# Performance work log

Hardware: AMD Instinct MI355X
Metric: run time of the kernel (lower is better)

## Reference

```python
import jax, jax.numpy as jnp
import numpy as np

DIST_THRESH = 0.1
W_DIST = 0.05
W_CHAMFER = 0.05
W_SEP = 0.0005


def setup_inputs() -> dict:
    key = jax.random.key(0)
    k1, k2, k3, k4 = jax.random.split(key, 4)
    B, N, K = 4, 200000, 64
    return {
        "landmarks_C": jax.random.uniform(k1, (B, N, 3), jnp.float32),          # predicted point coords
        "landmarks_F": jax.random.normal(k2, (B, N, 4), jnp.float32) * 0.05,    # [dist, dx, dy, dz]
        "targets_C": jax.random.uniform(k3, (B, K, 3), jnp.float32),            # GT landmark coords
        "targets_F": jax.random.randint(k4, (B, K), 0, 8),                      # GT landmark class labels
        "classes": jnp.arange(6),                                               # classes to supervise
    }


def reference(landmarks_C, landmarks_F, targets_C, targets_F, classes):
    def per_batch(C_i, F_i, tC, tF):
        # class mask over GT landmarks (replaces boolean indexing in torch)
        mask_k = jnp.any(tF[None, :] == classes[:, None], axis=0)          # [K]
        n_valid = mask_k.sum()
        dists_i = F_i[:, 0]                                                # predicted distance, [N]
        coords_i = C_i + F_i[:, 1:]                                        # refined coords, [N,3]
        # pairwise dists GT landmarks -> raw point coords, invalid classes pushed to +inf
        pd = jnp.linalg.norm(C_i[None, :, :] - tC[:, None, :], axis=-1)    # [K,N]
        pd = jnp.where(mask_k[:, None], pd, jnp.inf)
        min_d = pd.min(axis=0)                                             # [N]
        pm = min_d < DIST_THRESH                                           # points near some GT landmark
        # smooth-L1 (beta=1, sum) on predicted distance; clip(inf)=2*thresh reproduces empty-target fallback
        tgt = jnp.clip(min_d, 0.0, 2.0 * DIST_THRESH)
        diff = dists_i - tgt
        ad = jnp.abs(diff)
        dist_loss = jnp.where(ad < 1.0, 0.5 * diff * diff, ad - 0.5).sum()
        # pairwise dists GT landmarks -> refined coords
        ld = jnp.linalg.norm(coords_i[None, :, :] - tC[:, None, :], axis=-1)  # [K,N]
        ld_m = jnp.where(mask_k[:, None], ld, jnp.inf)
        p2g = jnp.where(pm, ld_m.min(axis=0), 0.0)                         # pred->gt, masked points only
        g2p = jnp.where(mask_k, ld_m.min(axis=1), 0.0)                     # gt->pred, valid GT only
        chamfer = (p2g * p2g).sum() + (g2p * g2p).sum()
        # separation: ratio of dists to 2 nearest (valid) GT landmarks, per masked point
        _, idx = jax.lax.top_k(-pd.T, 2)                                   # [N,2] indices of 2 smallest
        d01 = jnp.take_along_axis(ld.T, idx, axis=1)                       # [N,2]
        sep = jnp.where(pm, d01[:, 0] / d01[:, 1], 0.0).sum()
        sep = jnp.where(n_valid >= 2, sep, 0.0)
        return W_DIST * dist_loss + W_CHAMFER * chamfer + W_SEP * sep

    losses = jax.vmap(per_batch)(landmarks_C, landmarks_F, targets_C, targets_F)
    return losses.mean()
```

## Files before the change

kernel.cpp:

```cpp
#include <hip/hip_runtime.h>


constexpr int KT = 64;
constexpr int P  = 2;
constexpr float DIST_THRESH = 0.1f;
constexpr float W_DIST    = 0.05f;
constexpr float W_CHAMFER = 0.05f;
constexpr float W_SEP     = 0.0005f;
constexpr float PT_SENT = 1e18f;
constexpr float TG_SENT = -1e18f;
constexpr float BIGF = 3.0e38f;

__global__ void init_ws_kernel(unsigned int* g2p, float* sums, int ng, int ns) {
    int t = blockIdx.x * blockDim.x + threadIdx.x;
    if (t < ng) g2p[t] = 0x7F7FFFFFu;
    if (t < ns) sums[t] = 0.0f;
}

__global__ __launch_bounds__(256, 2)
void landmark_main(const float* __restrict__ C, const float* __restrict__ F,
                   const float* __restrict__ tC, const int* __restrict__ tF,
                   const int* __restrict__ classes, int n_classes,
                   int B, int N, int blocks_per_batch, int chunks_per_batch,
                   unsigned int* __restrict__ g2p_ws, float* __restrict__ sums)
{
    __shared__ float tx[KT], ty[KT], tz[KT];
    __shared__ float gredw[4][KT];
    __shared__ float rs[3][4];

    const int tid  = threadIdx.x;
    const int lane = tid & 63;
    const int wib  = tid >> 6;
    const int b    = blockIdx.x / blocks_per_batch;
    const int waves_per_batch = blocks_per_batch * (blockDim.x >> 6);
    const int wid  = (blockIdx.x - b * blocks_per_batch) * (blockDim.x >> 6) + wib;

    if (tid < KT) {
        int f = tF[b * KT + tid];
        bool valid = false;
        for (int c = 0; c < n_classes; ++c) valid = valid || (f == classes[c]);
        float x = TG_SENT, y = TG_SENT, z = TG_SENT;
        if (valid) {
            x = tC[(b * KT + tid) * 3 + 0];
            y = tC[(b * KT + tid) * 3 + 1];
            z = tC[(b * KT + tid) * 3 + 2];
        }
        tx[tid] = x; ty[tid] = y; tz[tid] = z;
    }
    __syncthreads();

    const float*  Cb = C + (size_t)b * N * 3;
    const float4* Fb = (const float4*)(F + (size_t)b * N * 4);

    float gmin = BIGF;
    float dist_acc = 0.f, p2g_acc = 0.f, sep_acc = 0.f;

    for (int chunk = wid; chunk < chunks_per_batch; chunk += waves_per_batch) {
        const int base = chunk * (64 * P);

        float px[P], py[P], pz[P], cx[P], cy[P], cz[P], f0[P];
        bool  vp[P];
        #pragma unroll
        for (int p = 0; p < P; ++p) {
            int n = base + p * 64 + lane;
            bool v = (n < N);
            vp[p] = v;
            int ni = v ? n : 0;
            float4 f4 = Fb[ni];
            float X = Cb[3 * ni + 0], Y = Cb[3 * ni + 1], Z = Cb[3 * ni + 2];
            f0[p] = f4.x;
            if (v) {
                px[p] = X;           py[p] = Y;           pz[p] = Z;
                cx[p] = X + f4.y;    cy[p] = Y + f4.z;    cz[p] = Z + f4.w;
            } else {
                px[p] = PT_SENT; py[p] = PT_SENT; pz[p] = PT_SENT;
                cx[p] = PT_SENT; cy[p] = PT_SENT; cz[p] = PT_SENT;
            }
        }

        float m1[P], m2[P], l1[P], l2[P], lmin[P];
        #pragma unroll
        for (int p = 0; p < P; ++p) {
            m1[p] = BIGF; m2[p] = BIGF; l1[p] = BIGF; l2[p] = BIGF; lmin[p] = BIGF;
        }

        int kk = lane;
        #pragma unroll 8
        for (int i = 0; i < 64; ++i) {
            float Tx = tx[kk], Ty = ty[kk], Tz = tz[kk];
            float dl = BIGF;
            #pragma unroll
            for (int p = 0; p < P; ++p) {
                float dx = px[p] - Tx, dy = py[p] - Ty, dz = pz[p] - Tz;
                float pd2 = fmaf(dz, dz, fmaf(dy, dy, dx * dx));
                float ex = cx[p] - Tx, ey = cy[p] - Ty, ez = cz[p] - Tz;
                float ld2 = fmaf(ez, ez, fmaf(ey, ey, ex * ex));
                bool c1 = pd2 < m1[p];
                bool c2 = pd2 < m2[p];
                m2[p] = c1 ? m1[p] : (c2 ? pd2 : m2[p]);
                l2[p] = c1 ? l1[p] : (c2 ? ld2 : l2[p]);
                m1[p] = c1 ? pd2 : m1[p];
                l1[p] = c1 ? ld2 : l1[p];
                lmin[p] = fminf(lmin[p], ld2);
                dl = fminf(dl, ld2);
            }
            float got = __shfl(dl, (lane - i) & 63, 64);
            gmin = fminf(gmin, got);
            kk = (kk + 1) & 63;
        }

        #pragma unroll
        for (int p = 0; p < P; ++p) {
            float mind = sqrtf(m1[p]);
            bool pm = mind < DIST_THRESH;
            float tgt = fminf(mind, 2.0f * DIST_THRESH);
            float diff = f0[p] - tgt;
            float ad = fabsf(diff);
            float sl1 = (ad < 1.0f) ? 0.5f * diff * diff : (ad - 0.5f);
            if (vp[p]) dist_acc += sl1;
            if (pm) {
                p2g_acc += lmin[p];
                sep_acc += sqrtf(l1[p]) / sqrtf(l2[p]);
            }
        }
    }

    float v0 = dist_acc, v1 = p2g_acc, v2 = sep_acc;
    #pragma unroll
    for (int o = 32; o > 0; o >>= 1) {
        v0 += __shfl_down(v0, o, 64);
        v1 += __shfl_down(v1, o, 64);
        v2 += __shfl_down(v2, o, 64);
    }
    if (lane == 0) { rs[0][wib] = v0; rs[1][wib] = v1; rs[2][wib] = v2; }
    gredw[wib][lane] = gmin;
    __syncthreads();

    const int nw = blockDim.x >> 6;
    if (tid < 3) {
        float s = 0.f;
        for (int w = 0; w < nw; ++w) s += rs[tid][w];
        atomicAdd(&sums[tid * B + b], s);
    }
    if (tid < KT) {
        float g = gredw[0][tid];
        for (int w = 1; w < nw; ++w) g = fminf(g, gredw[w][tid]);
        atomicMin(&g2p_ws[b * KT + tid], __float_as_uint(g));
    }
}

__global__ void landmark_finalize(const int* __restrict__ tF, const int* __restrict__ classes,
                                  int n_classes, const unsigned int* __restrict__ g2p_ws,
                                  const float* __restrict__ sums, float* __restrict__ out, int B)
{
    int tid = threadIdx.x;
    int b = tid >> 6, k = tid & 63;
    __shared__ float lossb[32];
    float g = 0.f, nv = 0.f;
    if (b < B) {
        int f = tF[b * KT + k];
        bool valid = false;
        for (int c = 0; c < n_classes; ++c) valid = valid || (f == classes[c]);
        if (valid) { nv = 1.f; g = __uint_as_float(g2p_ws[b * KT + k]); }
    }
    #pragma unroll
    for (int o = 32; o > 0; o >>= 1) {
        g  += __shfl_down(g, o, 64);
        nv += __shfl_down(nv, o, 64);
    }
    if (b < B && k == 0) {
        float sep = (nv >= 2.f) ? sums[2 * B + b] : 0.f;
        lossb[b] = W_DIST * sums[b] + W_CHAMFER * (sums[B + b] + g) + W_SEP * sep;
    }
    __syncthreads();
    if (tid == 0) {
        float s = 0.f;
        for (int i = 0; i < B; ++i) s += lossb[i];
        out[0] = s / (float)B;
    }
}

extern "C" void kernel_launch(void* const* d_in, const int* in_sizes, int n_in,
                              void* d_out, int out_size, void* d_ws, size_t ws_size,
                              hipStream_t stream)
{
    const float* C       = (const float*)d_in[0];
    const float* F       = (const float*)d_in[1];
    const float* tC      = (const float*)d_in[2];
    const int*   tF      = (const int*)d_in[3];
    const int*   classes = (const int*)d_in[4];
    const int n_classes = in_sizes[4];
    const int B = 4;
    const int N = in_sizes[0] / (3 * B);

    unsigned int* g2p_ws = (unsigned int*)d_ws;
    float* sums = (float*)((char*)d_ws + (size_t)B * KT * sizeof(unsigned int));

    init_ws_kernel<<<1, 512, 0, stream>>>(g2p_ws, sums, B * KT, 3 * B);

    const int bpb = 128;
    const int cpb = (N + 64 * P - 1) / (64 * P);
    landmark_main<<<bpb * B, 256, 0, stream>>>(C, F, tC, tF, classes, n_classes,
                                               B, N, bpb, cpb, g2p_ws, sums);
    landmark_finalize<<<1, B * 64, 0, stream>>>(tF, classes, n_classes, g2p_ws, sums,
                                                (float*)d_out, B);
}
```

Measured before the change: 118.5 us.

## Expand distance algebra, widen per-lane points, fuse finalize via last-block ticket

Rewrites the squared distances as |p|^2 - 2p·t + |t|^2 with targets packed as float4 in shared memory, and simplifies the top-2 tracking with min/max. Each lane now handles four points, and the grid is sized to one chunk per wave. The separate init and finalize kernels are replaced by memsets and a last-block ticket reduction. This reduces ALU work per point-target pair and launch overhead, at the cost of cancellation error in the expanded distance form and higher register pressure.

```diff
diff --git a/kernel.cpp b/kernel.cpp
--- a/kernel.cpp
+++ b/kernel.cpp
@@ -2,7 +2,7 @@
 
 
 constexpr int KT = 64;
-constexpr int P  = 2;
+constexpr int P  = 4;
 constexpr float DIST_THRESH = 0.1f;
 constexpr float W_DIST    = 0.05f;
 constexpr float W_CHAMFER = 0.05f;
@@ -11,29 +11,26 @@
 constexpr float TG_SENT = -1e18f;
 constexpr float BIGF = 3.0e38f;
 
-__global__ void init_ws_kernel(unsigned int* g2p, float* sums, int ng, int ns) {
-    int t = blockIdx.x * blockDim.x + threadIdx.x;
-    if (t < ng) g2p[t] = 0x7F7FFFFFu;
-    if (t < ns) sums[t] = 0.0f;
-}
-
-__global__ __launch_bounds__(256, 2)
-void landmark_main(const float* __restrict__ C, const float* __restrict__ F,
-                   const float* __restrict__ tC, const int* __restrict__ tF,
-                   const int* __restrict__ classes, int n_classes,
-                   int B, int N, int blocks_per_batch, int chunks_per_batch,
-                   unsigned int* __restrict__ g2p_ws, float* __restrict__ sums)
+__global__ __launch_bounds__(256, 4)
+void landmark_fused(const float* __restrict__ C, const float* __restrict__ F,
+                    const float* __restrict__ tC, const int* __restrict__ tF,
+                    const int* __restrict__ classes, int n_classes,
+                    int B, int N, int bpb, int cpb,
+                    unsigned int* __restrict__ g2p_ws, float* __restrict__ sums,
+                    unsigned int* __restrict__ ticket, float* __restrict__ out)
 {
-    __shared__ float tx[KT], ty[KT], tz[KT];
+    __shared__ float4 tgt[KT];
     __shared__ float gredw[4][KT];
     __shared__ float rs[3][4];
+    __shared__ int is_last;
+    __shared__ float lossb[4];
 
     const int tid  = threadIdx.x;
     const int lane = tid & 63;
     const int wib  = tid >> 6;
-    const int b    = blockIdx.x / blocks_per_batch;
-    const int waves_per_batch = blocks_per_batch * (blockDim.x >> 6);
-    const int wid  = (blockIdx.x - b * blocks_per_batch) * (blockDim.x >> 6) + wib;
+    const int b    = blockIdx.x / bpb;
+    const int waves_per_batch = bpb * 4;
+    const int wid  = (blockIdx.x - b * bpb) * 4 + wib;
 
     if (tid < KT) {
         int f = tF[b * KT + tid];
@@ -45,7 +42,8 @@
             y = tC[(b * KT + tid) * 3 + 1];
             z = tC[(b * KT + tid) * 3 + 2];
         }
-        tx[tid] = x; ty[tid] = y; tz[tid] = z;
+        tgt[tid] = make_float4(-2.f * x, -2.f * y, -2.f * z,
+                               x * x + y * y + z * z);
     }
     __syncthreads();
 
@@ -55,10 +53,10 @@
     float gmin = BIGF;
     float dist_acc = 0.f, p2g_acc = 0.f, sep_acc = 0.f;
 
-    for (int chunk = wid; chunk < chunks_per_batch; chunk += waves_per_batch) {
+    for (int chunk = wid; chunk < cpb; chunk += waves_per_batch) {
         const int base = chunk * (64 * P);
 
-        float px[P], py[P], pz[P], cx[P], cy[P], cz[P], f0[P];
+        float px[P], py[P], pz[P], pp[P], cx[P], cy[P], cz[P], cc[P], f0[P];
         bool  vp[P];
         #pragma unroll
         for (int p = 0; p < P; ++p) {
@@ -69,13 +67,12 @@
             float4 f4 = Fb[ni];
             float X = Cb[3 * ni + 0], Y = Cb[3 * ni + 1], Z = Cb[3 * ni + 2];
             f0[p] = f4.x;
-            if (v) {
-                px[p] = X;           py[p] = Y;           pz[p] = Z;
-                cx[p] = X + f4.y;    cy[p] = Y + f4.z;    cz[p] = Z + f4.w;
-            } else {
-                px[p] = PT_SENT; py[p] = PT_SENT; pz[p] = PT_SENT;
-                cx[p] = PT_SENT; cy[p] = PT_SENT; cz[p] = PT_SENT;
-            }
+            if (!v) { X = PT_SENT; Y = PT_SENT; Z = PT_SENT; f4.y = f4.z = f4.w = 0.f; }
+            px[p] = X;          py[p] = Y;          pz[p] = Z;
+            cx[p] = X + f4.y;   cy[p] = Y + f4.z;   cz[p] = Z + f4.w;
+            pp[p] = fmaf(X, X, fmaf(Y, Y, Z * Z)) + fmaf(f4.y, f4.y, 0.f) * 0.f;
+            pp[p] = fmaf(pz[p], pz[p], fmaf(py[p], py[p], px[p] * px[p]));
+            cc[p] = fmaf(cz[p], cz[p], fmaf(cy[p], cy[p], cx[p] * cx[p]));
         }
 
         float m1[P], m2[P], l1[P], l2[P], lmin[P];
@@ -85,21 +82,21 @@
         }
 
         int kk = lane;
-        #pragma unroll 8
+        #pragma unroll 4
         for (int i = 0; i < 64; ++i) {
-            float Tx = tx[kk], Ty = ty[kk], Tz = tz[kk];
+            float4 T = tgt[kk];
             float dl = BIGF;
             #pragma unroll
             for (int p = 0; p < P; ++p) {
-                float dx = px[p] - Tx, dy = py[p] - Ty, dz = pz[p] - Tz;
-                float pd2 = fmaf(dz, dz, fmaf(dy, dy, dx * dx));
-                float ex = cx[p] - Tx, ey = cy[p] - Ty, ez = cz[p] - Tz;
-                float ld2 = fmaf(ez, ez, fmaf(ey, ey, ex * ex));
+                float pd2 = fmaf(px[p], T.x, fmaf(py[p], T.y, fmaf(pz[p], T.z, pp[p] + T.w)));
+                float ld2 = fmaf(cx[p], T.x, fmaf(cy[p], T.y, fmaf(cz[p], T.z, cc[p] + T.w)));
                 bool c1 = pd2 < m1[p];
                 bool c2 = pd2 < m2[p];
-                m2[p] = c1 ? m1[p] : (c2 ? pd2 : m2[p]);
-                l2[p] = c1 ? l1[p] : (c2 ? ld2 : l2[p]);
-                m1[p] = c1 ? pd2 : m1[p];
+                float hi = fmaxf(m1[p], pd2);
+                m1[p] = fminf(m1[p], pd2);
+                m2[p] = fminf(m2[p], hi);
+                float tsel = c1 ? l1[p] : ld2;
+                l2[p] = c2 ? tsel : l2[p];
                 l1[p] = c1 ? ld2 : l1[p];
                 lmin[p] = fminf(lmin[p], ld2);
                 dl = fminf(dl, ld2);
@@ -111,16 +108,16 @@
 
         #pragma unroll
         for (int p = 0; p < P; ++p) {
-            float mind = sqrtf(m1[p]);
+            float mind = sqrtf(fmaxf(m1[p], 0.f));
             bool pm = mind < DIST_THRESH;
-            float tgt = fminf(mind, 2.0f * DIST_THRESH);
-            float diff = f0[p] - tgt;
+            float tgtv = fminf(mind, 2.0f * DIST_THRESH);
+            float diff = f0[p] - tgtv;
             float ad = fabsf(diff);
             float sl1 = (ad < 1.0f) ? 0.5f * diff * diff : (ad - 0.5f);
             if (vp[p]) dist_acc += sl1;
             if (pm) {
-                p2g_acc += lmin[p];
-                sep_acc += sqrtf(l1[p]) / sqrtf(l2[p]);
+                p2g_acc += fmaxf(lmin[p], 0.f);
+                sep_acc += sqrtf(fmaxf(l1[p], 0.f)) / sqrtf(fmaxf(l2[p], 1e-30f));
             }
         }
     }
@@ -136,47 +133,55 @@
     gredw[wib][lane] = gmin;
     __syncthreads();
 
-    const int nw = blockDim.x >> 6;
     if (tid < 3) {
-        float s = 0.f;
-        for (int w = 0; w < nw; ++w) s += rs[tid][w];
+        float s = rs[tid][0] + rs[tid][1] + rs[tid][2] + rs[tid][3];
         atomicAdd(&sums[tid * B + b], s);
     }
     if (tid < KT) {
-        float g = gredw[0][tid];
-        for (int w = 1; w < nw; ++w) g = fminf(g, gredw[w][tid]);
+        float g = fminf(fminf(gredw[0][tid], gredw[1][tid]),
+                        fminf(gredw[2][tid], gredw[3][tid]));
+        g = fmaxf(g, 0.f);
         atomicMin(&g2p_ws[b * KT + tid], __float_as_uint(g));
     }
-}
-
-__global__ void landmark_finalize(const int* __restrict__ tF, const int* __restrict__ classes,
-                                  int n_classes, const unsigned int* __restrict__ g2p_ws,
-                                  const float* __restrict__ sums, float* __restrict__ out, int B)
-{
-    int tid = threadIdx.x;
-    int b = tid >> 6, k = tid & 63;
-    __shared__ float lossb[32];
-    float g = 0.f, nv = 0.f;
-    if (b < B) {
-        int f = tF[b * KT + k];
-        bool valid = false;
-        for (int c = 0; c < n_classes; ++c) valid = valid || (f == classes[c]);
-        if (valid) { nv = 1.f; g = __uint_as_float(g2p_ws[b * KT + k]); }
-    }
-    #pragma unroll
-    for (int o = 32; o > 0; o >>= 1) {
-        g  += __shfl_down(g, o, 64);
-        nv += __shfl_down(nv, o, 64);
-    }
-    if (b < B && k == 0) {
-        float sep = (nv >= 2.f) ? sums[2 * B + b] : 0.f;
-        lossb[b] = W_DIST * sums[b] + W_CHAMFER * (sums[B + b] + g) + W_SEP * sep;
+
+    if (tid == 0) {
+        __threadfence();
+        unsigned int t = atomicAdd(ticket, 1u);
+        is_last = (t == (unsigned int)(gridDim.x - 1));
     }
     __syncthreads();
-    if (tid == 0) {
-        float s = 0.f;
-        for (int i = 0; i < B; ++i) s += lossb[i];
-        out[0] = s / (float)B;
+    if (!is_last) return;
+
+    {
+        const int fb = tid >> 6, fk = tid & 63;
+        float g = 0.f, nv = 0.f;
+        if (fb < B) {
+            int f = tF[fb * KT + fk];
+            bool valid = false;
+            for (int c = 0; c < n_classes; ++c) valid = valid || (f == classes[c]);
+            if (valid) {
+                nv = 1.f;
+                g = __uint_as_float(atomicMin(&g2p_ws[fb * KT + fk], 0xFFFFFFFFu));
+            }
+        }
+        #pragma unroll
+        for (int o = 32; o > 0; o >>= 1) {
+            g  += __shfl_down(g, o, 64);
+            nv += __shfl_down(nv, o, 64);
+        }
+        if (fb < B && fk == 0) {
+            float sd = atomicAdd(&sums[0 * B + fb], 0.f);
+            float sp = atomicAdd(&sums[1 * B + fb], 0.f);
+            float ss = atomicAdd(&sums[2 * B + fb], 0.f);
+            float sep = (nv >= 2.f) ? ss : 0.f;
+            lossb[fb] = W_DIST * sd + W_CHAMFER * (sp + g) + W_SEP * sep;
+        }
+        __syncthreads();
+        if (tid == 0) {
+            float s = 0.f;
+            for (int i = 0; i < B; ++i) s += lossb[i];
+            out[0] = s / (float)B;
+        }
     }
 }
 
@@ -194,14 +199,15 @@
     const int N = in_sizes[0] / (3 * B);
 
     unsigned int* g2p_ws = (unsigned int*)d_ws;
-    float* sums = (float*)((char*)d_ws + (size_t)B * KT * sizeof(unsigned int));
-
-    init_ws_kernel<<<1, 512, 0, stream>>>(g2p_ws, sums, B * KT, 3 * B);
-
-    const int bpb = 128;
+    float*        sums   = (float*)((char*)d_ws + KT * B * 4);
+    unsigned int* ticket = (unsigned int*)((char*)d_ws + KT * B * 4 + 12 * 4);
+
+    hipMemsetAsync(g2p_ws, 0x7F, KT * B * sizeof(unsigned int), stream);
+    hipMemsetAsync(sums, 0, 16 * sizeof(float), stream);
+
     const int cpb = (N + 64 * P - 1) / (64 * P);
-    landmark_main<<<bpb * B, 256, 0, stream>>>(C, F, tC, tF, classes, n_classes,
-                                               B, N, bpb, cpb, g2p_ws, sums);
-    landmark_finalize<<<1, B * 64, 0, stream>>>(tF, classes, n_classes, g2p_ws, sums,
-                                                (float*)d_out, B);
+    const int bpb = (cpb + 3) / 4;
+    landmark_fused<<<bpb * B, 256, 0, stream>>>(C, F, tC, tF, classes, n_classes,
+                                                B, N, bpb, cpb, g2p_ws, sums, ticket,
+                                                (float*)d_out);
 }
```

Result: faster. 112.0 us (-5.5%).
